# Kernel tuning notes

Measured on AMD Instinct MI355X. Metric: run time of the kernel, lower is better.

## Reference

```python
import jax, jax.numpy as jnp
import numpy as np

R = 200000
PAD = 14            # residue_pad_length (atom14)
ACD, ATD, RCD, RID = 32, 8, 32, 32
N_ATOM_CODES, N_ATOM_TYPES, N_RES_CODES = 38, 6, 21
MAX_SEQ = 1024
OUT_0E, OUT_1E = 128, 32
IN0 = PAD * ACD + PAD * ATD + RCD + RID  # 624 scalar (0e) input channels


def setup_inputs() -> dict:
    key = jax.random.key(0)
    ks = jax.random.split(key, 12)
    counts_np = (4 + (np.arange(R) % 11)).astype(np.int32)  # atoms per residue in [4,14]
    n_atoms = int(counts_np.sum())  # 1,799,991
    residue_index_atomwise = jnp.asarray(np.repeat(np.arange(R, dtype=np.int32), counts_np))
    return {
        "relative_coords": jax.random.normal(ks[0], (n_atoms, 3), dtype=jnp.float32),
        "atom_code_index": jax.random.randint(ks[1], (n_atoms,), 1, N_ATOM_CODES, dtype=jnp.int32),
        "atom_type_index": jax.random.randint(ks[2], (n_atoms,), 1, N_ATOM_TYPES, dtype=jnp.int32),
        "residue_index_atomwise": residue_index_atomwise,
        "counts": jnp.asarray(counts_np),
        "residue_code_index": jax.random.randint(ks[3], (R,), 1, N_RES_CODES, dtype=jnp.int32),
        "residue_sequence_index": jax.random.randint(ks[4], (R,), 0, MAX_SEQ, dtype=jnp.int32),
        "base_coords": jax.random.normal(ks[5], (R, 3), dtype=jnp.float32),
        "atom_code_table": jax.random.normal(ks[6], (N_ATOM_CODES, ACD), dtype=jnp.float32),
        "atom_type_table": jax.random.normal(ks[7], (N_ATOM_TYPES, ATD), dtype=jnp.float32),
        "residue_code_table": jax.random.normal(ks[8], (N_RES_CODES, RCD), dtype=jnp.float32),
        "residue_index_table": jax.random.normal(ks[9], (MAX_SEQ, RID), dtype=jnp.float32),
        "W0": jax.random.normal(ks[10], (IN0, OUT_0E), dtype=jnp.float32),
        "W1": jax.random.normal(ks[11], (PAD, OUT_1E), dtype=jnp.float32),
    }


def _ragged_to_padded(residue_index_atomwise, counts, relative_coords,
                      atom_code_index, atom_type_index):
    # Single O(atoms) scatter replacing the per-residue python loop.
    n_atoms = relative_coords.shape[0]
    nres = counts.shape[0]
    starts = jnp.concatenate([jnp.zeros((1,), counts.dtype), jnp.cumsum(counts)[:-1]])
    pos = jnp.arange(n_atoms, dtype=counts.dtype) - starts[residue_index_atomwise]
    mask = jnp.arange(PAD, dtype=counts.dtype)[None, :] < counts[:, None]  # [R, PAD]
    coords_pad = jnp.zeros((nres, PAD, 3), relative_coords.dtype).at[
        residue_index_atomwise, pos].set(relative_coords)
    codes_pad = jnp.zeros((nres, PAD), jnp.int32).at[residue_index_atomwise, pos].set(atom_code_index)
    types_pad = jnp.zeros((nres, PAD), jnp.int32).at[residue_index_atomwise, pos].set(atom_type_index)
    return coords_pad, codes_pad, types_pad, mask


def reference(relative_coords, atom_code_index, atom_type_index,
              residue_index_atomwise, counts, residue_code_index,
              residue_sequence_index, base_coords,
              atom_code_table, atom_type_table, residue_code_table,
              residue_index_table, W0, W1):
    nres = counts.shape[0]
    coords_pad, codes_pad, types_pad, mask = _ragged_to_padded(
        residue_index_atomwise, counts, relative_coords, atom_code_index, atom_type_index)
    # embedding lookups, masked at padded slots (as in the torch module)
    ac = atom_code_table[codes_pad] * mask[..., None]   # [R, PAD, ACD]
    at = atom_type_table[types_pad] * mask[..., None]   # [R, PAD, ATD]
    rc = residue_code_table[residue_code_index]         # [R, RCD]
    ri = residue_index_table[residue_sequence_index]    # [R, RID]
    scalars = jnp.concatenate(
        [ac.reshape(nres, -1), at.reshape(nres, -1), rc, ri], axis=-1)  # [R, IN0]
    # e3nn o3.Linear: per-irrep-type mixing with 1/sqrt(fan_in) normalization.
    y0 = (scalars @ W0) * (1.0 / jnp.sqrt(jnp.float32(IN0)))            # 0e -> 0e
    y1 = jnp.einsum('rmc,mn->rnc', coords_pad, W1) * (1.0 / jnp.sqrt(jnp.float32(PAD)))  # 1e -> 1e
    features = jnp.concatenate([y0, y1.reshape(nres, -1)], axis=-1)     # [R, 128 + 96]
    return base_coords, features
```

## Files before the change

kernel.cpp:

```cpp
#include <hip/hip_runtime.h>
#include <hip/hip_bf16.h>

#define PAD        14
#define ACD        32
#define ATD        8
#define RCD        32
#define RID        32
#define N_CODES    38
#define N_TYPES    6
#define NCT        (N_CODES * N_TYPES)
#define N_RES      21
#define MAX_SEQ    1024
#define IN0        624
#define OUT0       128
#define OUT1       32
#define FEAT       224

#define NROWS_TCT  (PAD * NCT)
#define ZROW       NROWS_TCT
#define ROW_RC0    (ZROW + 1)
#define ROW_RI0    (ROW_RC0 + N_RES)
#define NROWS_ALL  (ROW_RI0 + MAX_SEQ)

__device__ __constant__ const float NORM0 = 0.04003203845f;
__device__ __constant__ const float NORM1 = 0.26726124191f;

typedef float f32x2 __attribute__((ext_vector_type(2)));

#define SZ_W1N     (PAD * OUT1)

#define T2_SZ_TCT     (PAD * NCT * OUT0)
#define T2_OFF_TCT    0
#define T2_OFF_TRC    (T2_OFF_TCT + T2_SZ_TCT)
#define T2_SZ_TRC     (N_RES * OUT0)
#define T2_OFF_TRI    (T2_OFF_TRC + T2_SZ_TRC)
#define T2_SZ_TRI     (MAX_SEQ * OUT0)
#define T2_OFF_W1N    (T2_OFF_TRI + T2_SZ_TRI)
#define T2_OFF_STARTS (T2_OFF_W1N + SZ_W1N)

__device__ __forceinline__ unsigned short f2bf(float v) {
    __hip_bfloat16 h = __float2bfloat16(v);
    unsigned short u;
    __builtin_memcpy(&u, &h, 2);
    return u;
}
__device__ __forceinline__ float bf_lo(unsigned int d) { return __uint_as_float(d << 16); }
__device__ __forceinline__ float bf_hi(unsigned int d) { return __uint_as_float(d & 0xffff0000u); }

__global__ void build_starts(const int* __restrict__ resIdx, int n_atoms,
                             int* __restrict__ starts,
                             const float* __restrict__ baseIn,
                             float* __restrict__ outBase, int nbase) {
    int i = blockIdx.x * blockDim.x + threadIdx.x;
    if (i < nbase) outBase[i] = baseIn[i];
    if (i >= n_atoms) return;
    int r = resIdx[i];
    if (i == 0 || resIdx[i - 1] != r) starts[r] = i;
}

__global__ void build_tall(const float* __restrict__ act, const float* __restrict__ att,
                           const float* __restrict__ rct, const float* __restrict__ rit,
                           const float* __restrict__ W0, const float* __restrict__ W1,
                           __hip_bfloat16* __restrict__ Tall, float* __restrict__ W1n) {
    int b = blockIdx.x;
    int o = threadIdx.x;
    float acc = 0.f;
    if (b < NROWS_TCT) {
        int m = b / NCT, ct = b % NCT, c = ct / N_TYPES, t = ct % N_TYPES;
        const float* wc = W0 + (size_t)(m * ACD) * OUT0 + o;
        const float* wt = W0 + (size_t)(PAD * ACD + m * ATD) * OUT0 + o;
#pragma unroll
        for (int j = 0; j < ACD; ++j) acc += act[c * ACD + j] * wc[(size_t)j * OUT0];
#pragma unroll
        for (int j = 0; j < ATD; ++j) acc += att[t * ATD + j] * wt[(size_t)j * OUT0];
        Tall[(size_t)b * OUT0 + o] = __float2bfloat16(acc * NORM0);
    } else if (b == ZROW) {
        Tall[(size_t)b * OUT0 + o] = __float2bfloat16(0.f);
    } else if (b < ROW_RC0 + N_RES) {
        int c = b - ROW_RC0;
        const float* w = W0 + (size_t)(PAD * ACD + PAD * ATD) * OUT0 + o;
#pragma unroll
        for (int j = 0; j < RCD; ++j) acc += rct[c * RCD + j] * w[(size_t)j * OUT0];
        Tall[(size_t)b * OUT0 + o] = __float2bfloat16(acc * NORM0);
    } else if (b < NROWS_ALL) {
        int s = b - ROW_RI0;
        const float* w = W0 + (size_t)(PAD * ACD + PAD * ATD + RCD) * OUT0 + o;
#pragma unroll
        for (int j = 0; j < RID; ++j) acc += rit[s * RID + j] * w[(size_t)j * OUT0];
        Tall[(size_t)b * OUT0 + o] = __float2bfloat16(acc * NORM0);
    } else {
        for (int i = o; i < PAD * OUT1; i += OUT0) W1n[i] = W1[i] * NORM1;
    }
}

__global__ void build_meta(const int* __restrict__ starts, const int* __restrict__ counts,
                           const int* __restrict__ codeIdx, const int* __restrict__ typeIdx,
                           const float* __restrict__ coords,
                           const int* __restrict__ rcIdx, const int* __restrict__ rsIdx,
                           unsigned short* __restrict__ meta, int R) {
    int gid = blockIdx.x * blockDim.x + threadIdx.x;
    int r = gid >> 4, slot = gid & 15;
    if (r >= R) return;
    unsigned short* mp = meta + (size_t)r * 64;
    if (slot < PAD) {
        int cnt = counts[r];
        int row = ZROW;
        float cx = 0.f, cy = 0.f, cz = 0.f;
        if (slot < cnt) {
            int a = starts[r] + slot;
            row = slot * NCT + codeIdx[a] * N_TYPES + typeIdx[a];
            cx = coords[3 * (size_t)a + 0];
            cy = coords[3 * (size_t)a + 1];
            cz = coords[3 * (size_t)a + 2];
        }
        mp[slot]      = (unsigned short)row;
        mp[16 + slot] = f2bf(cx);
        mp[32 + slot] = f2bf(cy);
        mp[48 + slot] = f2bf(cz);
    } else if (slot == 14) {
        mp[14] = (unsigned short)(ROW_RC0 + rcIdx[r]);
    } else {
        mp[15] = (unsigned short)(ROW_RI0 + rsIdx[r]);
    }
}

__global__ __launch_bounds__(256) void main_fast(
    const int* __restrict__ meta32,
    const unsigned int* __restrict__ Tall,
    const float* __restrict__ W1n,
    float* __restrict__ outFeat, int R) {
    int lane   = threadIdx.x & 63;
    int lane32 = lane & 31;
    int wid    = threadIdx.x >> 6;
    int r = __builtin_amdgcn_readfirstlane(blockIdx.x * 4 + wid);
    if (r >= R) return;

    const int* mp = meta32 + (size_t)r * 32;
    int md[32];
#pragma unroll
    for (int j = 0; j < 32; ++j) md[j] = mp[j];

    float w14[PAD];
#pragma unroll
    for (int m = 0; m < PAD; ++m) w14[m] = W1n[m * OUT1 + lane32];

    unsigned int t[16];
#pragma unroll
    for (int k = 0; k < 8; ++k) {
        unsigned int dw = (unsigned int)md[k];
        unsigned int lo = dw & 0xffffu;
        unsigned int hi = dw >> 16;
        t[2 * k]     = Tall[(size_t)lo * 64 + lane];
        t[2 * k + 1] = Tall[(size_t)hi * 64 + lane];
    }

    float vx = 0.f, vy = 0.f, vz = 0.f;
#pragma unroll
    for (int m = 0; m < PAD; ++m) {
        int dw = m >> 1;
        unsigned int xd = (unsigned int)md[8 + dw];
        unsigned int yd = (unsigned int)md[16 + dw];
        unsigned int zd = (unsigned int)md[24 + dw];
        float cx = (m & 1) ? bf_hi(xd) : bf_lo(xd);
        float cy = (m & 1) ? bf_hi(yd) : bf_lo(yd);
        float cz = (m & 1) ? bf_hi(zd) : bf_lo(zd);
        vx = fmaf(cx, w14[m], vx);
        vy = fmaf(cy, w14[m], vy);
        vz = fmaf(cz, w14[m], vz);
    }

    float acx = 0.f, acy = 0.f;
#pragma unroll
    for (int j = 0; j < 16; ++j) {
        acx += bf_lo(t[j]);
        acy += bf_hi(t[j]);
    }

    float* fo = outFeat + (size_t)r * FEAT;
    f32x2 acc; acc.x = acx; acc.y = acy;
    __builtin_nontemporal_store(acc, reinterpret_cast<f32x2*>(fo) + lane);
    if (lane < 32) {
        float* p = fo + OUT0 + 3 * lane32;
        __builtin_nontemporal_store(vx, p + 0);
        __builtin_nontemporal_store(vy, p + 1);
        __builtin_nontemporal_store(vz, p + 2);
    }
}

__global__ void build_tables_t2(const float* __restrict__ act, const float* __restrict__ att,
                                const float* __restrict__ rct, const float* __restrict__ rit,
                                const float* __restrict__ W0, const float* __restrict__ W1,
                                float* __restrict__ Tct, float* __restrict__ Trc,
                                float* __restrict__ Tri, float* __restrict__ W1n) {
    int b = blockIdx.x;
    int o = threadIdx.x;
    float acc = 0.f;
    if (b < PAD * NCT) {
        int m = b / NCT, ct = b % NCT, c = ct / N_TYPES, t = ct % N_TYPES;
        const float* wc = W0 + (size_t)(m * ACD) * OUT0 + o;
        const float* wt = W0 + (size_t)(PAD * ACD + m * ATD) * OUT0 + o;
#pragma unroll
        for (int j = 0; j < ACD; ++j) acc += act[c * ACD + j] * wc[(size_t)j * OUT0];
#pragma unroll
        for (int j = 0; j < ATD; ++j) acc += att[t * ATD + j] * wt[(size_t)j * OUT0];
        Tct[(size_t)b * OUT0 + o] = acc * NORM0;
    } else if (b < PAD * NCT + N_RES) {
        int c = b - PAD * NCT;
        const float* w = W0 + (size_t)(PAD * ACD + PAD * ATD) * OUT0 + o;
#pragma unroll
        for (int j = 0; j < RCD; ++j) acc += rct[c * RCD + j] * w[(size_t)j * OUT0];
        Trc[(size_t)c * OUT0 + o] = acc * NORM0;
    } else if (b < PAD * NCT + N_RES + MAX_SEQ) {
        int s = b - (PAD * NCT + N_RES);
        const float* w = W0 + (size_t)(PAD * ACD + PAD * ATD + RCD) * OUT0 + o;
#pragma unroll
        for (int j = 0; j < RID; ++j) acc += rit[s * RID + j] * w[(size_t)j * OUT0];
        Tri[(size_t)s * OUT0 + o] = acc * NORM0;
    } else {
        for (int i = o; i < PAD * OUT1; i += OUT0) W1n[i] = W1[i] * NORM1;
    }
}

__global__ __launch_bounds__(256) void main_t2(
    const float*  __restrict__ coords, const int* __restrict__ codeIdx,
    const int*    __restrict__ typeIdx, const int* __restrict__ counts,
    const int*    __restrict__ rcIdx, const int* __restrict__ rsIdx,
    const float*  __restrict__ W1n,
    const float*  __restrict__ Tct, const float* __restrict__ Trc,
    const float*  __restrict__ Tri, const int* __restrict__ starts,
    float* __restrict__ outFeat, int R, int n_atoms) {
    int wid  = threadIdx.x >> 6;
    int lane = threadIdx.x & 63;
    int r = __builtin_amdgcn_readfirstlane(blockIdx.x * 4 + wid);
    if (r >= R) return;
    int start = starts[r];
    int cnt   = counts[r];
    int rc    = rcIdx[r];
    int rs    = rsIdx[r];
    int lane32 = lane & 31;
    int ci = 1, ti = 1;
    float crd = 0.f;
    if (lane < PAD) {
        int a = min(start + lane, n_atoms - 1);
        ci = codeIdx[a];
        ti = typeIdx[a];
    }
    if (lane < 3 * PAD) {
        int i3 = min(start * 3 + lane, 3 * n_atoms - 1);
        crd = coords[i3];
    }
    const f32x2* Tct2 = reinterpret_cast<const f32x2*>(Tct);
    const f32x2* Trc2 = reinterpret_cast<const f32x2*>(Trc);
    const f32x2* Tri2 = reinterpret_cast<const f32x2*>(Tri);
    f32x2 a0 = Trc2[(size_t)rc * 64 + lane];
    f32x2 a1 = Tri2[(size_t)rs * 64 + lane];
    int cmax = max(cnt - 1, 0);
    f32x2 t[PAD];
#pragma unroll
    for (int m = 0; m < PAD; ++m) {
        int mm = min(m, cmax);
        int cd = __builtin_amdgcn_readlane(ci, mm);
        int tp = __builtin_amdgcn_readlane(ti, mm);
        t[m] = Tct2[(size_t)(mm * NCT + cd * N_TYPES + tp) * 64 + lane];
    }
    float acx = a0.x + a1.x;
    float acy = a0.y + a1.y;
    float vx = 0.f, vy = 0.f, vz = 0.f;
#pragma unroll
    for (int m = 0; m < PAD; ++m) {
        int mm = min(m, cmax);
        float msk = (m < cnt) ? 1.f : 0.f;
        acx = fmaf(t[m].x, msk, acx);
        acy = fmaf(t[m].y, msk, acy);
        float cx = __uint_as_float(__builtin_amdgcn_readlane(__float_as_uint(crd), 3 * mm + 0));
        float cy = __uint_as_float(__builtin_amdgcn_readlane(__float_as_uint(crd), 3 * mm + 1));
        float cz = __uint_as_float(__builtin_amdgcn_readlane(__float_as_uint(crd), 3 * mm + 2));
        float w  = W1n[m * OUT1 + lane32] * msk;
        vx = fmaf(cx, w, vx);
        vy = fmaf(cy, w, vy);
        vz = fmaf(cz, w, vz);
    }
    float* fo = outFeat + (size_t)r * FEAT;
    f32x2 accv; accv.x = acx; accv.y = acy;
    __builtin_nontemporal_store(accv, reinterpret_cast<f32x2*>(fo) + lane);
    if (lane < 32) {
        float* p = fo + OUT0 + 3 * lane32;
        __builtin_nontemporal_store(vx, p + 0);
        __builtin_nontemporal_store(vy, p + 1);
        __builtin_nontemporal_store(vz, p + 2);
    }
}

__global__ __launch_bounds__(128) void fallback_kernel(
    const float* __restrict__ coords, const int* __restrict__ codeIdx,
    const int* __restrict__ typeIdx, const int* __restrict__ resIdx,
    const int* __restrict__ counts, const int* __restrict__ rcIdx,
    const int* __restrict__ rsIdx, const float* __restrict__ baseIn,
    const float* __restrict__ act, const float* __restrict__ att,
    const float* __restrict__ rct, const float* __restrict__ rit,
    const float* __restrict__ W0, const float* __restrict__ W1,
    float* __restrict__ outBase, float* __restrict__ outFeat, int R, int n_atoms) {
    int r = blockIdx.x, tid = threadIdx.x;
    __shared__ float s[IN0];
    __shared__ int sh_start;
    if (tid == 0) {
        int lo = 0, hi = n_atoms;
        while (lo < hi) { int mid = (lo + hi) >> 1; if (resIdx[mid] < r) lo = mid + 1; else hi = mid; }
        sh_start = lo;
    }
    __syncthreads();
    int start = sh_start, cnt = counts[r];
    for (int j = tid; j < IN0; j += 128) {
        float v = 0.f;
        if (j < PAD * ACD) {
            int m = j >> 5, jj = j & 31;
            if (m < cnt) v = act[codeIdx[start + m] * ACD + jj];
        } else if (j < PAD * ACD + PAD * ATD) {
            int t = j - PAD * ACD; int m = t >> 3, jj = t & 7;
            if (m < cnt) v = att[typeIdx[start + m] * ATD + jj];
        } else if (j < PAD * ACD + PAD * ATD + RCD) {
            v = rct[rcIdx[r] * RCD + (j - PAD * ACD - PAD * ATD)];
        } else {
            v = rit[rsIdx[r] * RID + (j - PAD * ACD - PAD * ATD - RCD)];
        }
        s[j] = v;
    }
    __syncthreads();
    float accv = 0.f;
    for (int j = 0; j < IN0; ++j) accv += s[j] * W0[(size_t)j * OUT0 + tid];
    float* fo = outFeat + (size_t)r * FEAT;
    fo[tid] = accv * NORM0;
    if (tid < 96) {
        int n = tid / 3, c = tid % 3;
        float v = 0.f;
        for (int m = 0; m < cnt; ++m) v += coords[(size_t)(start + m) * 3 + c] * W1[m * OUT1 + n];
        fo[OUT0 + tid] = v * NORM1;
    }
    if (tid < 3) outBase[(size_t)r * 3 + tid] = baseIn[(size_t)r * 3 + tid];
}

extern "C" void kernel_launch(void* const* d_in, const int* in_sizes, int n_in,
                              void* d_out, int out_size, void* d_ws, size_t ws_size,
                              hipStream_t stream) {
    const float* coords = (const float*)d_in[0];
    const int*   codeIdx = (const int*)d_in[1];
    const int*   typeIdx = (const int*)d_in[2];
    const int*   resIdx  = (const int*)d_in[3];
    const int*   counts  = (const int*)d_in[4];
    const int*   rcIdx   = (const int*)d_in[5];
    const int*   rsIdx   = (const int*)d_in[6];
    const float* baseIn  = (const float*)d_in[7];
    const float* act     = (const float*)d_in[8];
    const float* att     = (const float*)d_in[9];
    const float* rct     = (const float*)d_in[10];
    const float* rit     = (const float*)d_in[11];
    const float* W0      = (const float*)d_in[12];
    const float* W1      = (const float*)d_in[13];

    int n_atoms = in_sizes[1];
    int R       = in_sizes[4];

    float* out     = (float*)d_out;
    float* outBase = out;
    float* outFeat = out + (size_t)R * 3;

    size_t tallBytes = (size_t)NROWS_ALL * OUT0 * 2;
    size_t w1nOff    = tallBytes;
    size_t startsOff = w1nOff + (size_t)SZ_W1N * 4;
    size_t metaOff   = (startsOff + (size_t)R * 4 + 255) & ~(size_t)255;
    size_t needFast  = metaOff + (size_t)R * 128;
    size_t needT2    = (size_t)(T2_OFF_STARTS + R) * 4;

    if (ws_size >= needFast) {
        char* wsb = (char*)d_ws;
        __hip_bfloat16* Tall   = (__hip_bfloat16*)wsb;
        unsigned int*   TallU  = (unsigned int*)wsb;
        float*          W1n    = (float*)(wsb + w1nOff);
        int*            starts = (int*)(wsb + startsOff);
        unsigned short* meta   = (unsigned short*)(wsb + metaOff);
        int*            meta32 = (int*)(wsb + metaOff);

        build_starts<<<(n_atoms + 255) / 256, 256, 0, stream>>>(
            resIdx, n_atoms, starts, baseIn, outBase, R * 3);
        build_tall<<<NROWS_ALL + 1, OUT0, 0, stream>>>(
            act, att, rct, rit, W0, W1, Tall, W1n);
        build_meta<<<((size_t)R * 16 + 255) / 256, 256, 0, stream>>>(
            starts, counts, codeIdx, typeIdx, coords, rcIdx, rsIdx, meta, R);
        main_fast<<<(R + 3) / 4, 256, 0, stream>>>(meta32, TallU, W1n, outFeat, R);
    } else if (ws_size >= needT2) {
        float* ws     = (float*)d_ws;
        float* Tct    = ws + T2_OFF_TCT;
        float* Trc    = ws + T2_OFF_TRC;
        float* Tri    = ws + T2_OFF_TRI;
        float* W1n    = ws + T2_OFF_W1N;
        int*   starts = (int*)(ws + T2_OFF_STARTS);
        build_starts<<<(n_atoms + 255) / 256, 256, 0, stream>>>(
            resIdx, n_atoms, starts, baseIn, outBase, R * 3);
        int nrows = PAD * NCT + N_RES + MAX_SEQ + 1;
        build_tables_t2<<<nrows, OUT0, 0, stream>>>(act, att, rct, rit, W0, W1,
                                                    Tct, Trc, Tri, W1n);
        main_t2<<<(R + 3) / 4, 256, 0, stream>>>(
            coords, codeIdx, typeIdx, counts, rcIdx, rsIdx, W1n,
            Tct, Trc, Tri, starts, outFeat, R, n_atoms);
    } else {
        fallback_kernel<<<R, 128, 0, stream>>>(
            coords, codeIdx, typeIdx, resIdx, counts, rcIdx, rsIdx, baseIn,
            act, att, rct, rit, W0, W1, outBase, outFeat, R, n_atoms);
    }
}
```

Baseline: 89.94 us.

## Fuse table build with meta build and process two residues per wave

Folds the table-building kernel and the per-residue metadata kernel into one launch. Table blocks use 128 of 256 threads, and the remaining blocks build the metadata. The main kernel now handles two residues per wavefront, which halves the grid, issues more independent gathers per wave and amortises the W1 weight loads. The cost is higher register pressure from 64 metadata words and 32 table values per thread, which may lower occupancy.

```diff
diff --git a/kernel.cpp b/kernel.cpp
--- a/kernel.cpp
+++ b/kernel.cpp
@@ -58,47 +58,50 @@
     if (i == 0 || resIdx[i - 1] != r) starts[r] = i;
 }
 
-__global__ void build_tall(const float* __restrict__ act, const float* __restrict__ att,
-                           const float* __restrict__ rct, const float* __restrict__ rit,
-                           const float* __restrict__ W0, const float* __restrict__ W1,
-                           __hip_bfloat16* __restrict__ Tall, float* __restrict__ W1n) {
+__global__ void build_tall_meta(
+    const float* __restrict__ act, const float* __restrict__ att,
+    const float* __restrict__ rct, const float* __restrict__ rit,
+    const float* __restrict__ W0, const float* __restrict__ W1,
+    __hip_bfloat16* __restrict__ Tall, float* __restrict__ W1n,
+    const int* __restrict__ starts, const int* __restrict__ counts,
+    const int* __restrict__ codeIdx, const int* __restrict__ typeIdx,
+    const float* __restrict__ coords,
+    const int* __restrict__ rcIdx, const int* __restrict__ rsIdx,
+    unsigned short* __restrict__ meta, int R) {
     int b = blockIdx.x;
-    int o = threadIdx.x;
-    float acc = 0.f;
-    if (b < NROWS_TCT) {
-        int m = b / NCT, ct = b % NCT, c = ct / N_TYPES, t = ct % N_TYPES;
-        const float* wc = W0 + (size_t)(m * ACD) * OUT0 + o;
-        const float* wt = W0 + (size_t)(PAD * ACD + m * ATD) * OUT0 + o;
-#pragma unroll
-        for (int j = 0; j < ACD; ++j) acc += act[c * ACD + j] * wc[(size_t)j * OUT0];
-#pragma unroll
-        for (int j = 0; j < ATD; ++j) acc += att[t * ATD + j] * wt[(size_t)j * OUT0];
-        Tall[(size_t)b * OUT0 + o] = __float2bfloat16(acc * NORM0);
-    } else if (b == ZROW) {
-        Tall[(size_t)b * OUT0 + o] = __float2bfloat16(0.f);
-    } else if (b < ROW_RC0 + N_RES) {
-        int c = b - ROW_RC0;
-        const float* w = W0 + (size_t)(PAD * ACD + PAD * ATD) * OUT0 + o;
-#pragma unroll
-        for (int j = 0; j < RCD; ++j) acc += rct[c * RCD + j] * w[(size_t)j * OUT0];
-        Tall[(size_t)b * OUT0 + o] = __float2bfloat16(acc * NORM0);
-    } else if (b < NROWS_ALL) {
-        int s = b - ROW_RI0;
-        const float* w = W0 + (size_t)(PAD * ACD + PAD * ATD + RCD) * OUT0 + o;
-#pragma unroll
-        for (int j = 0; j < RID; ++j) acc += rit[s * RID + j] * w[(size_t)j * OUT0];
-        Tall[(size_t)b * OUT0 + o] = __float2bfloat16(acc * NORM0);
-    } else {
-        for (int i = o; i < PAD * OUT1; i += OUT0) W1n[i] = W1[i] * NORM1;
-    }
-}
-
-__global__ void build_meta(const int* __restrict__ starts, const int* __restrict__ counts,
-                           const int* __restrict__ codeIdx, const int* __restrict__ typeIdx,
-                           const float* __restrict__ coords,
-                           const int* __restrict__ rcIdx, const int* __restrict__ rsIdx,
-                           unsigned short* __restrict__ meta, int R) {
-    int gid = blockIdx.x * blockDim.x + threadIdx.x;
+    if (b <= NROWS_ALL) {
+        int o = threadIdx.x;
+        if (o >= OUT0) return;
+        float acc = 0.f;
+        if (b < NROWS_TCT) {
+            int m = b / NCT, ct = b % NCT, c = ct / N_TYPES, t = ct % N_TYPES;
+            const float* wc = W0 + (size_t)(m * ACD) * OUT0 + o;
+            const float* wt = W0 + (size_t)(PAD * ACD + m * ATD) * OUT0 + o;
+#pragma unroll
+            for (int j = 0; j < ACD; ++j) acc += act[c * ACD + j] * wc[(size_t)j * OUT0];
+#pragma unroll
+            for (int j = 0; j < ATD; ++j) acc += att[t * ATD + j] * wt[(size_t)j * OUT0];
+            Tall[(size_t)b * OUT0 + o] = __float2bfloat16(acc * NORM0);
+        } else if (b == ZROW) {
+            Tall[(size_t)b * OUT0 + o] = __float2bfloat16(0.f);
+        } else if (b < ROW_RC0 + N_RES) {
+            int c = b - ROW_RC0;
+            const float* w = W0 + (size_t)(PAD * ACD + PAD * ATD) * OUT0 + o;
+#pragma unroll
+            for (int j = 0; j < RCD; ++j) acc += rct[c * RCD + j] * w[(size_t)j * OUT0];
+            Tall[(size_t)b * OUT0 + o] = __float2bfloat16(acc * NORM0);
+        } else if (b < NROWS_ALL) {
+            int s = b - ROW_RI0;
+            const float* w = W0 + (size_t)(PAD * ACD + PAD * ATD + RCD) * OUT0 + o;
+#pragma unroll
+            for (int j = 0; j < RID; ++j) acc += rit[s * RID + j] * w[(size_t)j * OUT0];
+            Tall[(size_t)b * OUT0 + o] = __float2bfloat16(acc * NORM0);
+        } else {
+            for (int i = o; i < PAD * OUT1; i += OUT0) W1n[i] = W1[i] * NORM1;
+        }
+        return;
+    }
+    int gid = (b - (NROWS_ALL + 1)) * 256 + threadIdx.x;
     int r = gid >> 4, slot = gid & 15;
     if (r >= R) return;
     unsigned short* mp = meta + (size_t)r * 64;
@@ -124,7 +127,7 @@
     }
 }
 
-__global__ __launch_bounds__(256) void main_fast(
+__global__ __launch_bounds__(256) void main_fast2(
     const int* __restrict__ meta32,
     const unsigned int* __restrict__ Tall,
     const float* __restrict__ W1n,
@@ -132,58 +135,95 @@
     int lane   = threadIdx.x & 63;
     int lane32 = lane & 31;
     int wid    = threadIdx.x >> 6;
-    int r = __builtin_amdgcn_readfirstlane(blockIdx.x * 4 + wid);
-    if (r >= R) return;
-
-    const int* mp = meta32 + (size_t)r * 32;
-    int md[32];
+    int pr = __builtin_amdgcn_readfirstlane(blockIdx.x * 4 + wid);
+    int r0 = pr * 2;
+    if (r0 >= R) return;
+    bool has1 = (r0 + 1) < R;
+
+    float w14[PAD];
+#pragma unroll
+    for (int m = 0; m < PAD; ++m) w14[m] = W1n[m * OUT1 + lane32];
+
+    const int* mp = meta32 + (size_t)r0 * 32;
+    int md[64];
 #pragma unroll
     for (int j = 0; j < 32; ++j) md[j] = mp[j];
-
-    float w14[PAD];
-#pragma unroll
-    for (int m = 0; m < PAD; ++m) w14[m] = W1n[m * OUT1 + lane32];
-
-    unsigned int t[16];
+    if (has1) {
+#pragma unroll
+        for (int j = 32; j < 64; ++j) md[j] = mp[j];
+    } else {
+#pragma unroll
+        for (int j = 32; j < 64; ++j) md[j] = 0;
+    }
+
+    unsigned int t0[16], t1[16];
 #pragma unroll
     for (int k = 0; k < 8; ++k) {
         unsigned int dw = (unsigned int)md[k];
-        unsigned int lo = dw & 0xffffu;
-        unsigned int hi = dw >> 16;
-        t[2 * k]     = Tall[(size_t)lo * 64 + lane];
-        t[2 * k + 1] = Tall[(size_t)hi * 64 + lane];
-    }
-
-    float vx = 0.f, vy = 0.f, vz = 0.f;
+        t0[2 * k]     = Tall[(size_t)(dw & 0xffffu) * 64 + lane];
+        t0[2 * k + 1] = Tall[(size_t)(dw >> 16) * 64 + lane];
+    }
+    if (has1) {
+#pragma unroll
+        for (int k = 0; k < 8; ++k) {
+            unsigned int dw = (unsigned int)md[32 + k];
+            t1[2 * k]     = Tall[(size_t)(dw & 0xffffu) * 64 + lane];
+            t1[2 * k + 1] = Tall[(size_t)(dw >> 16) * 64 + lane];
+        }
+    }
+
+    float vx0 = 0.f, vy0 = 0.f, vz0 = 0.f;
+    float vx1 = 0.f, vy1 = 0.f, vz1 = 0.f;
 #pragma unroll
     for (int m = 0; m < PAD; ++m) {
         int dw = m >> 1;
-        unsigned int xd = (unsigned int)md[8 + dw];
-        unsigned int yd = (unsigned int)md[16 + dw];
-        unsigned int zd = (unsigned int)md[24 + dw];
-        float cx = (m & 1) ? bf_hi(xd) : bf_lo(xd);
-        float cy = (m & 1) ? bf_hi(yd) : bf_lo(yd);
-        float cz = (m & 1) ? bf_hi(zd) : bf_lo(zd);
-        vx = fmaf(cx, w14[m], vx);
-        vy = fmaf(cy, w14[m], vy);
-        vz = fmaf(cz, w14[m], vz);
-    }
-
-    float acx = 0.f, acy = 0.f;
-#pragma unroll
-    for (int j = 0; j < 16; ++j) {
-        acx += bf_lo(t[j]);
-        acy += bf_hi(t[j]);
-    }
-
-    float* fo = outFeat + (size_t)r * FEAT;
-    f32x2 acc; acc.x = acx; acc.y = acy;
-    __builtin_nontemporal_store(acc, reinterpret_cast<f32x2*>(fo) + lane);
+        unsigned int xd0 = (unsigned int)md[8 + dw];
+        unsigned int yd0 = (unsigned int)md[16 + dw];
+        unsigned int zd0 = (unsigned int)md[24 + dw];
+        float cx0 = (m & 1) ? bf_hi(xd0) : bf_lo(xd0);
+        float cy0 = (m & 1) ? bf_hi(yd0) : bf_lo(yd0);
+        float cz0 = (m & 1) ? bf_hi(zd0) : bf_lo(zd0);
+        vx0 = fmaf(cx0, w14[m], vx0);
+        vy0 = fmaf(cy0, w14[m], vy0);
+        vz0 = fmaf(cz0, w14[m], vz0);
+        unsigned int xd1 = (unsigned int)md[40 + dw];
+        unsigned int yd1 = (unsigned int)md[48 + dw];
+        unsigned int zd1 = (unsigned int)md[56 + dw];
+        float cx1 = (m & 1) ? bf_hi(xd1) : bf_lo(xd1);
+        float cy1 = (m & 1) ? bf_hi(yd1) : bf_lo(yd1);
+        float cz1 = (m & 1) ? bf_hi(zd1) : bf_lo(zd1);
+        vx1 = fmaf(cx1, w14[m], vx1);
+        vy1 = fmaf(cy1, w14[m], vy1);
+        vz1 = fmaf(cz1, w14[m], vz1);
+    }
+
+    float acx0 = 0.f, acy0 = 0.f;
+#pragma unroll
+    for (int j = 0; j < 16; ++j) { acx0 += bf_lo(t0[j]); acy0 += bf_hi(t0[j]); }
+
+    float* fo0 = outFeat + (size_t)r0 * FEAT;
+    f32x2 a0; a0.x = acx0; a0.y = acy0;
+    __builtin_nontemporal_store(a0, reinterpret_cast<f32x2*>(fo0) + lane);
     if (lane < 32) {
-        float* p = fo + OUT0 + 3 * lane32;
-        __builtin_nontemporal_store(vx, p + 0);
-        __builtin_nontemporal_store(vy, p + 1);
-        __builtin_nontemporal_store(vz, p + 2);
+        float* p = fo0 + OUT0 + 3 * lane32;
+        __builtin_nontemporal_store(vx0, p + 0);
+        __builtin_nontemporal_store(vy0, p + 1);
+        __builtin_nontemporal_store(vz0, p + 2);
+    }
+
+    if (has1) {
+        float acx1 = 0.f, acy1 = 0.f;
+#pragma unroll
+        for (int j = 0; j < 16; ++j) { acx1 += bf_lo(t1[j]); acy1 += bf_hi(t1[j]); }
+        float* fo1 = fo0 + FEAT;
+        f32x2 a1; a1.x = acx1; a1.y = acy1;
+        __builtin_nontemporal_store(a1, reinterpret_cast<f32x2*>(fo1) + lane);
+        if (lane < 32) {
+            float* p = fo1 + OUT0 + 3 * lane32;
+            __builtin_nontemporal_store(vx1, p + 0);
+            __builtin_nontemporal_store(vy1, p + 1);
+            __builtin_nontemporal_store(vz1, p + 2);
+        }
     }
 }
 
@@ -382,11 +422,13 @@
 
         build_starts<<<(n_atoms + 255) / 256, 256, 0, stream>>>(
             resIdx, n_atoms, starts, baseIn, outBase, R * 3);
-        build_tall<<<NROWS_ALL + 1, OUT0, 0, stream>>>(
-            act, att, rct, rit, W0, W1, Tall, W1n);
-        build_meta<<<((size_t)R * 16 + 255) / 256, 256, 0, stream>>>(
+        int metaBlocks = (int)(((size_t)R * 16 + 255) / 256);
+        build_tall_meta<<<(NROWS_ALL + 1) + metaBlocks, 256, 0, stream>>>(
+            act, att, rct, rit, W0, W1, Tall, W1n,
             starts, counts, codeIdx, typeIdx, coords, rcIdx, rsIdx, meta, R);
-        main_fast<<<(R + 3) / 4, 256, 0, stream>>>(meta32, TallU, W1n, outFeat, R);
+        int pairs = (R + 1) / 2;
+        main_fast2<<<(pairs + 3) / 4, 256, 0, stream>>>(
+            meta32, TallU, W1n, outFeat, R);
     } else if (ws_size >= needT2) {
         float* ws     = (float*)d_ws;
         float* Tct    = ws + T2_OFF_TCT;
```

After: 80.66 us. 1.12x faster.
